# Performance work log

Measured on AMD Instinct MI355X. Metric: run time of the kernel, lower is better.

## Reference

```python
import jax, jax.numpy as jnp
import numpy as np

N = 2048          # num nodes (all graphs in batch)
F = 64            # in_channels (per-feature MLPs)
C = 8             # out_channels
H = 32            # hidden_channels
G = 16            # num graphs


def setup_inputs() -> dict:
    key = jax.random.key(0)
    ks = jax.random.split(key, 12)
    x = jax.random.normal(ks[0], (N, F), dtype=jnp.float32)
    dist = jax.random.uniform(ks[1], (N, N), dtype=jnp.float32)
    norm = jax.random.uniform(ks[2], (N, N), dtype=jnp.float32)
    batch = jnp.sort(jax.random.randint(ks[3], (N,), 0, G))
    # per-feature MLPs (F independent 2-layer MLPs, input dim 1)
    fs_W1 = jax.random.normal(ks[4], (F, H), dtype=jnp.float32)    # Linear(1,H).weight squeezed
    fs_b1 = jnp.zeros((F, H), dtype=jnp.float32)
    fs_W2 = jax.random.normal(ks[5], (F, C, H), dtype=jnp.float32) * (1.0 / np.sqrt(H))
    fs_b2 = jnp.zeros((F, C), dtype=jnp.float32)
    # rho MLP (scalar distance -> C weights)
    rho_W1 = jax.random.normal(ks[6], (H,), dtype=jnp.float32)     # Linear(1,H).weight squeezed
    rho_b1 = jnp.zeros((H,), dtype=jnp.float32)
    rho_W2 = jax.random.normal(ks[7], (C, H), dtype=jnp.float32) * (1.0 / np.sqrt(H))
    rho_b2 = jnp.zeros((C,), dtype=jnp.float32)
    return {
        "x": x, "dist": dist, "norm": norm, "batch": batch,
        "fs_W1": fs_W1, "fs_b1": fs_b1, "fs_W2": fs_W2, "fs_b2": fs_b2,
        "rho_W1": rho_W1, "rho_b1": rho_b1, "rho_W2": rho_W2, "rho_b2": rho_b2,
    }


def reference(x, dist, norm, batch, fs_W1, fs_b1, fs_W2, fs_b2,
              rho_W1, rho_b1, rho_W2, rho_b2):
    # per-feature MLPs: fx[n,f,c] = MLP_f(x[n,f])
    h = jax.nn.relu(x[:, :, None] * fs_W1[None] + fs_b1[None])          # [N,F,H]
    fx = jnp.einsum('nfh,fch->nfc', h, fs_W2) + fs_b2[None]             # [N,F,C]
    f_sum = fx.sum(axis=1)                                              # [N,C]

    # rho MLP over inverse distances (dense N x N)
    inv_dist = 1.0 / (1.0 + dist)                                       # [N,N]
    rh = jax.nn.relu(inv_dist[:, :, None] * rho_W1 + rho_b1)            # [N,N,H]
    rho = jnp.einsum('ijh,ch->ijc', rh, rho_W2) + rho_b2                # [N,N,C]

    # normalize (zeros in norm -> 1)
    norm_safe = jnp.where(norm == 0.0, 1.0, norm)
    rho = rho / norm_safe[:, :, None]

    # block-diagonal batch mask
    mask = (batch[:, None] == batch[None, :])                           # [N,N]
    rho = rho * mask[:, :, None]

    out = jnp.einsum('ijc,jc->ic', rho, f_sum)                          # [N,C]

    # graph-level readout
    graph_out = jax.ops.segment_sum(out, batch, num_segments=G)         # [G,C]
    return graph_out
```

## Files before the change

kernel.cpp:

```cpp
#include <hip/hip_runtime.h>

#define N_NODES 2048
#define F_IN 64
#define C_OUT 8
#define H_HID 32
#define G_NUM 16

__global__ __launch_bounds__(256) void fsum_bounds_kernel(
    const float* __restrict__ x, const float* __restrict__ W1,
    const float* __restrict__ b1, const float* __restrict__ W2,
    const float* __restrict__ b2, float* __restrict__ fsum,
    const int* __restrict__ batch, int* __restrict__ starts,
    float* __restrict__ out)
{
    const int tid = threadIdx.x;

    if (blockIdx.x >= 256) {
        for (int i = tid; i < N_NODES; i += 256) {
            const int cur  = batch[i];
            const int prev = (i == 0) ? -1 : batch[i - 1];
            for (int g = prev + 1; g <= cur; ++g) starts[g] = i;
            if (i == N_NODES - 1)
                for (int g = cur + 1; g <= G_NUM; ++g) starts[g] = N_NODES;
        }
        if (tid < G_NUM * C_OUT) out[tid] = 0.0f;
        return;
    }

    __shared__ float sA[H_HID * 256];
    __shared__ float sB[H_HID * 256];
    float* tmp = sA;

    #pragma unroll
    for (int k = 0; k < 8; ++k) {
        const int e  = tid + k * 256;
        const int f_ = e >> 5, h_ = e & 31;
        tmp[h_ * 65 + f_]        = W1[e];
        tmp[2080 + h_ * 65 + f_] = b1[e];
    }
    __syncthreads();

    const int wv = tid >> 6;
    const int f  = tid & 63;
    float w1r[H_HID], b1r[H_HID];
    #pragma unroll
    for (int h = 0; h < H_HID; ++h) {
        w1r[h] = tmp[h * 65 + f];
        b1r[h] = tmp[2080 + h * 65 + f];
    }
    __syncthreads();

    #pragma unroll
    for (int k = 0; k < 16; ++k) {
        const int q = tid + k * 256;
        const float4 v = *(const float4*)&W2[4 * q];
        const int h0 = (q & 7) * 4;
        const int c  = (q >> 3) & 7;
        const int ff = q >> 6;
        float* dst = (c < 4) ? sA : sB;
        const int col = (ff * 4 + (c & 3)) ^ ((q & 7) << 2);
        dst[(h0 + 0) * 256 + col] = v.x;
        dst[(h0 + 1) * 256 + col] = v.y;
        dst[(h0 + 2) * 256 + col] = v.z;
        dst[(h0 + 3) * 256 + col] = v.w;
    }
    __syncthreads();

    const int n0 = blockIdx.x * 8 + wv * 2;
    const float xv0 = x[n0 * F_IN + f];
    const float xv1 = x[n0 * F_IN + F_IN + f];

    float4 a00 = {0,0,0,0}, a01 = {0,0,0,0};
    float4 a10 = {0,0,0,0}, a11 = {0,0,0,0};

    #pragma unroll
    for (int h = 0; h < H_HID; ++h) {
        const float rv0 = fmaxf(fmaf(xv0, w1r[h], b1r[h]), 0.f);
        const float rv1 = fmaxf(fmaf(xv1, w1r[h], b1r[h]), 0.f);
        const int colx = (4 * f) ^ ((h >> 2) << 2);
        const float4 wa = *(const float4*)&sA[h * 256 + colx];
        const float4 wb = *(const float4*)&sB[h * 256 + colx];
        a00.x = fmaf(rv0, wa.x, a00.x); a00.y = fmaf(rv0, wa.y, a00.y);
        a00.z = fmaf(rv0, wa.z, a00.z); a00.w = fmaf(rv0, wa.w, a00.w);
        a01.x = fmaf(rv0, wb.x, a01.x); a01.y = fmaf(rv0, wb.y, a01.y);
        a01.z = fmaf(rv0, wb.z, a01.z); a01.w = fmaf(rv0, wb.w, a01.w);
        a10.x = fmaf(rv1, wa.x, a10.x); a10.y = fmaf(rv1, wa.y, a10.y);
        a10.z = fmaf(rv1, wa.z, a10.z); a10.w = fmaf(rv1, wa.w, a10.w);
        a11.x = fmaf(rv1, wb.x, a11.x); a11.y = fmaf(rv1, wb.y, a11.y);
        a11.z = fmaf(rv1, wb.z, a11.z); a11.w = fmaf(rv1, wb.w, a11.w);
    }
    const float4 b2lo = *(const float4*)&b2[f * C_OUT];
    const float4 b2hi = *(const float4*)&b2[f * C_OUT + 4];
    a00.x += b2lo.x; a00.y += b2lo.y; a00.z += b2lo.z; a00.w += b2lo.w;
    a01.x += b2hi.x; a01.y += b2hi.y; a01.z += b2hi.z; a01.w += b2hi.w;
    a10.x += b2lo.x; a10.y += b2lo.y; a10.z += b2lo.z; a10.w += b2lo.w;
    a11.x += b2hi.x; a11.y += b2hi.y; a11.z += b2hi.z; a11.w += b2hi.w;

    float v0[C_OUT] = {a00.x,a00.y,a00.z,a00.w,a01.x,a01.y,a01.z,a01.w};
    float v1[C_OUT] = {a10.x,a10.y,a10.z,a10.w,a11.x,a11.y,a11.z,a11.w};
    #pragma unroll
    for (int c = 0; c < C_OUT; ++c) {
        float s0 = v0[c], s1 = v1[c];
        for (int off = 32; off; off >>= 1) {
            s0 += __shfl_down(s0, off);
            s1 += __shfl_down(s1, off);
        }
        v0[c] = s0; v1[c] = s1;
    }
    if (f == 0) {
        *(float4*)&fsum[n0 * C_OUT]           = make_float4(v0[0],v0[1],v0[2],v0[3]);
        *(float4*)&fsum[n0 * C_OUT + 4]       = make_float4(v0[4],v0[5],v0[6],v0[7]);
        *(float4*)&fsum[(n0 + 1) * C_OUT]     = make_float4(v1[0],v1[1],v1[2],v1[3]);
        *(float4*)&fsum[(n0 + 1) * C_OUT + 4] = make_float4(v1[4],v1[5],v1[6],v1[7]);
    }
}

__global__ __launch_bounds__(256) void row_readout_kernel(
    const float* __restrict__ dist, const float* __restrict__ norm,
    const int* __restrict__ batch, const int* __restrict__ starts,
    const float* __restrict__ rW1, const float* __restrict__ rb1,
    const float* __restrict__ rW2, const float* __restrict__ rb2,
    const float* __restrict__ fsum, float* __restrict__ out)
{
    const int tid = threadIdx.x;

    __shared__ float sW1[H_HID], sb1[H_HID], sW2[C_OUT * H_HID], sb2[C_OUT];
    __shared__ float sRow[4][C_OUT];
    __shared__ int   sG[4];
    if (tid < H_HID) { sW1[tid] = rW1[tid]; sb1[tid] = rb1[tid]; }
    if (tid >= 64 && tid < 64 + C_OUT) sb2[tid - 64] = rb2[tid - 64];
    if (tid >= 128) { const int k = tid - 128;
        sW2[k] = rW2[k]; sW2[k + 128] = rW2[k + 128]; }
    __syncthreads();

    const int wv = tid >> 6, lane = tid & 63;
    const int i = blockIdx.x * 4 + wv;
    const int g = batch[i];
    const int js = starts[g];
    const int je = starts[g + 1];

    float acc[C_OUT] = {0.f,0.f,0.f,0.f,0.f,0.f,0.f,0.f};

    for (int j = js + lane; j < je; j += 64) {
        const float d  = dist[i * N_NODES + j];
        const float s  = 1.0f / (1.0f + d);
        const float nv = norm[i * N_NODES + j];
        const float invn = (nv == 0.0f) ? 1.0f : (1.0f / nv);

        float rho[C_OUT];
        #pragma unroll
        for (int c = 0; c < C_OUT; ++c) rho[c] = sb2[c];

        #pragma unroll
        for (int h = 0; h < H_HID; ++h) {
            const float rh = fmaxf(fmaf(s, sW1[h], sb1[h]), 0.f);
            #pragma unroll
            for (int c = 0; c < C_OUT; ++c)
                rho[c] = fmaf(rh, sW2[c * H_HID + h], rho[c]);
        }

        const float4 f0 = *(const float4*)&fsum[j * C_OUT];
        const float4 f1 = *(const float4*)&fsum[j * C_OUT + 4];
        acc[0] = fmaf(rho[0] * invn, f0.x, acc[0]);
        acc[1] = fmaf(rho[1] * invn, f0.y, acc[1]);
        acc[2] = fmaf(rho[2] * invn, f0.z, acc[2]);
        acc[3] = fmaf(rho[3] * invn, f0.w, acc[3]);
        acc[4] = fmaf(rho[4] * invn, f1.x, acc[4]);
        acc[5] = fmaf(rho[5] * invn, f1.y, acc[5]);
        acc[6] = fmaf(rho[6] * invn, f1.z, acc[6]);
        acc[7] = fmaf(rho[7] * invn, f1.w, acc[7]);
    }

    #pragma unroll
    for (int c = 0; c < C_OUT; ++c) {
        float v = acc[c];
        for (int off = 32; off; off >>= 1) v += __shfl_down(v, off);
        acc[c] = v;
    }
    if (lane == 0) {
        *(float4*)&sRow[wv][0] = make_float4(acc[0],acc[1],acc[2],acc[3]);
        *(float4*)&sRow[wv][4] = make_float4(acc[4],acc[5],acc[6],acc[7]);
        sG[wv] = g;
    }
    __syncthreads();

    if (tid < C_OUT) {
        const int c  = tid;
        const int gF = sG[0], gL = sG[3];
        for (int gg = gF; gg <= gL; ++gg) {
            float s = 0.f;
            bool any = false;
            #pragma unroll
            for (int r = 0; r < 4; ++r)
                if (sG[r] == gg) { s += sRow[r][c]; any = true; }
            if (any) unsafeAtomicAdd(&out[gg * C_OUT + c], s);
        }
    }
}

extern "C" void kernel_launch(void* const* d_in, const int* in_sizes, int n_in,
                              void* d_out, int out_size, void* d_ws, size_t ws_size,
                              hipStream_t stream)
{
    const float* x    = (const float*)d_in[0];
    const float* dist = (const float*)d_in[1];
    const float* norm = (const float*)d_in[2];
    const int*   batch= (const int*)d_in[3];
    const float* fsW1 = (const float*)d_in[4];
    const float* fsb1 = (const float*)d_in[5];
    const float* fsW2 = (const float*)d_in[6];
    const float* fsb2 = (const float*)d_in[7];
    const float* rW1  = (const float*)d_in[8];
    const float* rb1  = (const float*)d_in[9];
    const float* rW2  = (const float*)d_in[10];
    const float* rb2  = (const float*)d_in[11];
    float* out = (float*)d_out;

    float* fsum   = (float*)d_ws;
    int*   starts = (int*)(fsum + N_NODES * C_OUT);

    fsum_bounds_kernel<<<257, 256, 0, stream>>>(x, fsW1, fsb1, fsW2, fsb2,
                                                fsum, batch, starts, out);
    row_readout_kernel<<<N_NODES / 4, 256, 0, stream>>>(dist, norm, batch, starts,
                                                        rW1, rb1, rW2, rb2,
                                                        fsum, out);
}
```

Baseline: 23.62 us.

## Column-chunk decomposition with last-block deterministic readout reduction

Replaces the per-row readout kernel with a grid of 64 column chunks by 8 row groups. Each block caches its 32 fsum columns in shared memory and loops over the graphs its chunk spans. Per-graph partial sums go to a workspace buffer, and the last block to finish (found through an atomic counter) reduces them into the output, replacing float atomics. The aim is better load balance and determinism. The cost is strided 32-wide column reads of dist and norm, half-idle lanes on chunks that cross graph boundaries, and a serial final reduction done by one block.

Result: slower. 43.77 us (+85.3%).

```diff
diff --git a/kernel.cpp b/kernel.cpp
--- a/kernel.cpp
+++ b/kernel.cpp
@@ -5,13 +5,19 @@
 #define C_OUT 8
 #define H_HID 32
 #define G_NUM 16
+#define CHUNK 32
+#define NCB   64
+#define NRB   8
+#define NBLK2 (NCB * NRB)
+#define AL(p)    __hip_atomic_load((p),  __ATOMIC_RELAXED, __HIP_MEMORY_SCOPE_AGENT)
+#define AS(p,v)  __hip_atomic_store((p), (v), __ATOMIC_RELAXED, __HIP_MEMORY_SCOPE_AGENT)
 
 __global__ __launch_bounds__(256) void fsum_bounds_kernel(
     const float* __restrict__ x, const float* __restrict__ W1,
     const float* __restrict__ b1, const float* __restrict__ W2,
     const float* __restrict__ b2, float* __restrict__ fsum,
     const int* __restrict__ batch, int* __restrict__ starts,
-    float* __restrict__ out)
+    int* __restrict__ counter)
 {
     const int tid = threadIdx.x;
 
@@ -23,7 +29,7 @@
             if (i == N_NODES - 1)
                 for (int g = cur + 1; g <= G_NUM; ++g) starts[g] = N_NODES;
         }
-        if (tid < G_NUM * C_OUT) out[tid] = 0.0f;
+        if (tid == 0) counter[0] = 0;
         return;
     }
 
@@ -72,7 +78,6 @@
 
     float4 a00 = {0,0,0,0}, a01 = {0,0,0,0};
     float4 a10 = {0,0,0,0}, a11 = {0,0,0,0};
-
     #pragma unroll
     for (int h = 0; h < H_HID; ++h) {
         const float rv0 = fmaxf(fmaf(xv0, w1r[h], b1r[h]), 0.f);
@@ -115,86 +120,121 @@
     }
 }
 
-__global__ __launch_bounds__(256) void row_readout_kernel(
+__global__ __launch_bounds__(256) void colsum_readout_kernel(
     const float* __restrict__ dist, const float* __restrict__ norm,
     const int* __restrict__ batch, const int* __restrict__ starts,
     const float* __restrict__ rW1, const float* __restrict__ rb1,
     const float* __restrict__ rW2, const float* __restrict__ rb2,
-    const float* __restrict__ fsum, float* __restrict__ out)
+    const float* __restrict__ fsum, float* part, int* counter,
+    float* __restrict__ out)
 {
+    __shared__ float sW1[H_HID], sb1[H_HID], sW2[C_OUT * H_HID], sb2[C_OUT];
+    __shared__ float sFs[C_OUT * CHUNK];
+    __shared__ float sRed[4][C_OUT];
+    __shared__ int   sStarts[G_NUM + 1];
+    __shared__ int   sWin;
+    __shared__ float sAcc[256];
+
     const int tid = threadIdx.x;
-
-    __shared__ float sW1[H_HID], sb1[H_HID], sW2[C_OUT * H_HID], sb2[C_OUT];
-    __shared__ float sRow[4][C_OUT];
-    __shared__ int   sG[4];
+    const int b   = blockIdx.x;
+    const int cb  = b >> 3, rb = b & 7;
+    const int j0  = cb * CHUNK;
+    const int wv  = tid >> 6, lane = tid & 63;
+
     if (tid < H_HID) { sW1[tid] = rW1[tid]; sb1[tid] = rb1[tid]; }
     if (tid >= 64 && tid < 64 + C_OUT) sb2[tid - 64] = rb2[tid - 64];
+    if (tid >= 96 && tid < 96 + G_NUM + 1) sStarts[tid - 96] = starts[tid - 96];
     if (tid >= 128) { const int k = tid - 128;
         sW2[k] = rW2[k]; sW2[k + 128] = rW2[k + 128]; }
-    __syncthreads();
-
-    const int wv = tid >> 6, lane = tid & 63;
-    const int i = blockIdx.x * 4 + wv;
-    const int g = batch[i];
-    const int js = starts[g];
-    const int je = starts[g + 1];
-
-    float acc[C_OUT] = {0.f,0.f,0.f,0.f,0.f,0.f,0.f,0.f};
-
-    for (int j = js + lane; j < je; j += 64) {
-        const float d  = dist[i * N_NODES + j];
-        const float s  = 1.0f / (1.0f + d);
-        const float nv = norm[i * N_NODES + j];
-        const float invn = (nv == 0.0f) ? 1.0f : (1.0f / nv);
-
-        float rho[C_OUT];
+    {
+        const int jj = tid >> 3, c = tid & 7;
+        sFs[c * CHUNK + jj] = fsum[(j0 + jj) * C_OUT + c];
+    }
+    __syncthreads();
+
+    const int gs = batch[j0], ge = batch[j0 + CHUNK - 1];
+    const int jj = lane & 31, hf = lane >> 5;
+    const int j  = j0 + jj;
+
+    for (int g = gs; g <= ge; ++g) {
+        const int is = sStarts[g], ie = sStarts[g + 1];
+        const int jlo = max(j0, is), jhi = min(j0 + CHUNK, ie);
+        const bool actj = (j >= jlo) && (j < jhi);
+        const int glen = ie - is;
+
+        float acc[C_OUT] = {0,0,0,0,0,0,0,0};
+        for (int r = rb * 8 + wv * 2 + hf; r < glen; r += 64) {
+            if (actj) {
+                const int i = is + r;
+                const float d  = dist[i * N_NODES + j];
+                const float s  = 1.0f / (1.0f + d);
+                const float nv = norm[i * N_NODES + j];
+                const float invn = (nv == 0.0f) ? 1.0f : (1.0f / nv);
+
+                float rho[C_OUT];
+                #pragma unroll
+                for (int c = 0; c < C_OUT; ++c) rho[c] = sb2[c];
+                #pragma unroll
+                for (int h = 0; h < H_HID; ++h) {
+                    const float rh = fmaxf(fmaf(s, sW1[h], sb1[h]), 0.f);
+                    #pragma unroll
+                    for (int c = 0; c < C_OUT; ++c)
+                        rho[c] = fmaf(rh, sW2[c * H_HID + h], rho[c]);
+                }
+                #pragma unroll
+                for (int c = 0; c < C_OUT; ++c)
+                    acc[c] = fmaf(rho[c] * invn, sFs[c * CHUNK + jj], acc[c]);
+            }
+        }
+
         #pragma unroll
-        for (int c = 0; c < C_OUT; ++c) rho[c] = sb2[c];
-
-        #pragma unroll
-        for (int h = 0; h < H_HID; ++h) {
-            const float rh = fmaxf(fmaf(s, sW1[h], sb1[h]), 0.f);
+        for (int c = 0; c < C_OUT; ++c) {
+            float v = acc[c];
+            for (int off = 32; off; off >>= 1) v += __shfl_down(v, off);
+            acc[c] = v;
+        }
+        if (lane == 0) {
             #pragma unroll
-            for (int c = 0; c < C_OUT; ++c)
-                rho[c] = fmaf(rh, sW2[c * H_HID + h], rho[c]);
-        }
-
-        const float4 f0 = *(const float4*)&fsum[j * C_OUT];
-        const float4 f1 = *(const float4*)&fsum[j * C_OUT + 4];
-        acc[0] = fmaf(rho[0] * invn, f0.x, acc[0]);
-        acc[1] = fmaf(rho[1] * invn, f0.y, acc[1]);
-        acc[2] = fmaf(rho[2] * invn, f0.z, acc[2]);
-        acc[3] = fmaf(rho[3] * invn, f0.w, acc[3]);
-        acc[4] = fmaf(rho[4] * invn, f1.x, acc[4]);
-        acc[5] = fmaf(rho[5] * invn, f1.y, acc[5]);
-        acc[6] = fmaf(rho[6] * invn, f1.z, acc[6]);
-        acc[7] = fmaf(rho[7] * invn, f1.w, acc[7]);
-    }
-
-    #pragma unroll
-    for (int c = 0; c < C_OUT; ++c) {
-        float v = acc[c];
-        for (int off = 32; off; off >>= 1) v += __shfl_down(v, off);
-        acc[c] = v;
-    }
-    if (lane == 0) {
-        *(float4*)&sRow[wv][0] = make_float4(acc[0],acc[1],acc[2],acc[3]);
-        *(float4*)&sRow[wv][4] = make_float4(acc[4],acc[5],acc[6],acc[7]);
-        sG[wv] = g;
-    }
-    __syncthreads();
-
-    if (tid < C_OUT) {
-        const int c  = tid;
-        const int gF = sG[0], gL = sG[3];
-        for (int gg = gF; gg <= gL; ++gg) {
-            float s = 0.f;
-            bool any = false;
-            #pragma unroll
-            for (int r = 0; r < 4; ++r)
-                if (sG[r] == gg) { s += sRow[r][c]; any = true; }
-            if (any) unsafeAtomicAdd(&out[gg * C_OUT + c], s);
-        }
+            for (int c = 0; c < C_OUT; ++c) sRed[wv][c] = acc[c];
+        }
+        __syncthreads();
+        if (tid < C_OUT) {
+            const float s4 = sRed[0][tid] + sRed[1][tid]
+                           + sRed[2][tid] + sRed[3][tid];
+            AS(&part[(g * NBLK2 + b) * C_OUT + tid], s4);
+        }
+        __syncthreads();
+    }
+
+    __syncthreads();
+    if (tid == 0) {
+        const int old = __hip_atomic_fetch_add(counter, 1, __ATOMIC_RELAXED,
+                                               __HIP_MEMORY_SCOPE_AGENT);
+        sWin = (old == NBLK2 - 1) ? 1 : 0;
+    }
+    __syncthreads();
+    if (!sWin) return;
+
+    for (int g = 0; g < G_NUM; ++g) {
+        const int is = sStarts[g], ie = sStarts[g + 1];
+        if (is >= ie) {
+            if (tid < C_OUT) out[g * C_OUT + tid] = 0.0f;
+            __syncthreads();
+            continue;
+        }
+        const int bLo = (is >> 5) * NRB;
+        const int bHi = (((ie - 1) >> 5) + 1) * NRB;
+        float t = 0.0f;
+        for (int b2 = bLo + (tid >> 3); b2 < bHi; b2 += 32)
+            t += AL(&part[(g * NBLK2 + b2) * C_OUT + (tid & 7)]);
+        sAcc[tid] = t;
+        __syncthreads();
+        if (tid < C_OUT) {
+            float s = 0.0f;
+            for (int p = 0; p < 32; ++p) s += sAcc[p * C_OUT + tid];
+            out[g * C_OUT + tid] = s;
+        }
+        __syncthreads();
     }
 }
 
@@ -216,12 +256,14 @@
     const float* rb2  = (const float*)d_in[11];
     float* out = (float*)d_out;
 
-    float* fsum   = (float*)d_ws;
-    int*   starts = (int*)(fsum + N_NODES * C_OUT);
+    float* fsum    = (float*)d_ws;
+    int*   starts  = (int*)(fsum + N_NODES * C_OUT);
+    int*   counter = starts + 32;
+    float* part    = (float*)(counter + 32);
 
     fsum_bounds_kernel<<<257, 256, 0, stream>>>(x, fsW1, fsb1, fsW2, fsb2,
-                                                fsum, batch, starts, out);
-    row_readout_kernel<<<N_NODES / 4, 256, 0, stream>>>(dist, norm, batch, starts,
-                                                        rW1, rb1, rW2, rb2,
-                                                        fsum, out);
+                                                fsum, batch, starts, counter);
+    colsum_readout_kernel<<<NBLK2, 256, 0, stream>>>(dist, norm, batch, starts,
+                                                     rW1, rb1, rW2, rb2,
+                                                     fsum, part, counter, out);
 }
```
